# Kernel optimization log

Hardware: AMD Instinct MI355X
Metric: run time of the kernel (lower is better)

Reference implementation:

```python
import jax, jax.numpy as jnp
import numpy as np

N_NODES = 50000


def _gin_aggregate(x, src, dst):
    # sum_{j in N(i)} x_j via scatter-add over edges; eps=0 so add self term
    msg = x[src]  # [E, d]
    return x + jax.ops.segment_sum(msg, dst, num_segments=N_NODES)


def _mlp(h, Wa, ba, Wb, bb):
    return jax.nn.relu(h @ Wa + ba) @ Wb + bb


def setup_inputs() -> dict:
    key = jax.random.key(0)
    ks = jax.random.split(key, 12)
    d_in, d_h, n_cls, n_edges = 128, 128, 40, 800000
    x = jax.random.normal(ks[0], (N_NODES, d_in), dtype=jnp.float32)
    edge_index = jax.random.randint(ks[1], (2, n_edges), 0, N_NODES, dtype=jnp.int64)
    s = lambda k, sh: jax.random.normal(k, sh, dtype=jnp.float32) / np.sqrt(sh[0])
    return {
        "x": x,
        "edge_index": edge_index,
        "W11": s(ks[2], (d_in, 2 * d_h)), "b11": jnp.zeros((2 * d_h,), jnp.float32),
        "W12": s(ks[3], (2 * d_h, d_h)), "b12": jnp.zeros((d_h,), jnp.float32),
        "W21": s(ks[4], (d_h, 2 * d_h)), "b21": jnp.zeros((2 * d_h,), jnp.float32),
        "W22": s(ks[5], (2 * d_h, d_h)), "b22": jnp.zeros((d_h,), jnp.float32),
        "Wfc": s(ks[6], (d_h, n_cls)), "bfc": jnp.zeros((n_cls,), jnp.float32),
    }


def reference(x, edge_index, W11, b11, W12, b12, W21, b21, W22, b22, Wfc, bfc):
    src, dst = edge_index[0], edge_index[1]
    # GINConv 1: aggregate then MLP, followed by ReLU
    h = _mlp(_gin_aggregate(x, src, dst), W11, b11, W12, b12)
    h = jax.nn.relu(h)
    # GINConv 2
    h = _mlp(_gin_aggregate(h, src, dst), W21, b21, W22, b22)
    h = jax.nn.relu(h)
    # final classifier
    return h @ Wfc + bfc
```

## Files before the change

kernel.cpp:

```cpp
#include <hip/hip_runtime.h>

#define N_NODES 50000
#define N_EDGES 800000
#define NBUCK   98
#define EPB     2048
#define NSB     391
#define BCAP    64
#define CAPB    12288

typedef __attribute__((ext_vector_type(8))) short short8;
typedef __attribute__((ext_vector_type(4))) float floatx4;

__device__ __forceinline__ float b2f(unsigned short u) {
    union { unsigned int i; float f; } v;
    v.i = ((unsigned int)u) << 16;
    return v.f;
}
__device__ __forceinline__ float ubits(unsigned int b) {
    union { unsigned int i; float f; } v;
    v.i = b;
    return v.f;
}
__device__ __forceinline__ unsigned short f2b(float f) {
    union { float f; unsigned int i; } v;
    v.f = f;
    unsigned int r = v.i + 0x7FFFu + ((v.i >> 16) & 1u);
    return (unsigned short)(r >> 16);
}

__global__ __launch_bounds__(256) void prep_scatter(
    const float* __restrict__ x,
    const float* __restrict__ W11, const float* __restrict__ W12,
    const float* __restrict__ W21, const float* __restrict__ W22,
    const float* __restrict__ Wfc,
    const int* __restrict__ srcv, const int* __restrict__ dstv,
    unsigned short* __restrict__ xb,
    unsigned short* __restrict__ Wt11, unsigned short* __restrict__ Wt12,
    unsigned short* __restrict__ Wt21, unsigned short* __restrict__ Wt22,
    unsigned short* __restrict__ Wfct,
    int* __restrict__ cnt, int* __restrict__ tmp) {
    const int bid = blockIdx.x;
    const int tid = threadIdx.x;
    if (bid < NSB) {
        __shared__ int hist[NBUCK];
        const int k = bid;
        const int e0 = k * EPB;
        for (int i = tid; i < NBUCK; i += 256) hist[i] = 0;
        __syncthreads();
#pragma unroll
        for (int j = 0; j < EPB / 256; ++j) {
            int e = e0 + j * 256 + tid;
            if (e < N_EDGES) atomicAdd(&hist[dstv[e] >> 9], 1);
        }
        __syncthreads();
        for (int i = tid; i < NBUCK; i += 256) {
            cnt[i * NSB + k] = hist[i];
            hist[i] = 0;
        }
        __syncthreads();
#pragma unroll
        for (int j = 0; j < EPB / 256; ++j) {
            int e = e0 + j * 256 + tid;
            if (e < N_EDGES) {
                int d = dstv[e];
                int b = d >> 9;
                int r = atomicAdd(&hist[b], 1);
                if (r < BCAP)
                    tmp[((size_t)k * NBUCK + b) * BCAP + r] = srcv[e] | ((d & 511) << 16);
            }
        }
    } else if (bid < NSB + 512) {
        int wb = bid - NSB;
        int which = wb >> 7;
        int idx = (wb & 127) * 256 + tid;
        const float* W = (which == 0) ? W11 : (which == 1) ? W12 : (which == 2) ? W21 : W22;
        unsigned short* Wt = (which == 0) ? Wt11 : (which == 1) ? Wt12 : (which == 2) ? Wt21 : Wt22;
        int K = (which & 1) ? 256 : 128;
        int N = (which & 1) ? 128 : 256;
        int k = idx / N, n = idx - k * N;
        Wt[n * K + k] = f2b(W[idx]);
    } else if (bid < NSB + 536) {
        int idx = (bid - NSB - 512) * 256 + tid;
        int n = idx >> 7, k = idx & 127;
        Wfct[idx] = (n < 40) ? f2b(Wfc[k * 40 + n]) : (unsigned short)0;
    } else {
        int i = (bid - NSB - 536) * 256 + tid;
        const float4 a = *reinterpret_cast<const float4*>(x + (size_t)i * 8);
        const float4 b = *reinterpret_cast<const float4*>(x + (size_t)i * 8 + 4);
        ushort4 u0, u1;
        u0.x = f2b(a.x); u0.y = f2b(a.y); u0.z = f2b(a.z); u0.w = f2b(a.w);
        u1.x = f2b(b.x); u1.y = f2b(b.y); u1.z = f2b(b.z); u1.w = f2b(b.w);
        *reinterpret_cast<ushort4*>(xb + (size_t)i * 8) = u0;
        *reinterpret_cast<ushort4*>(xb + (size_t)i * 8 + 4) = u1;
    }
}

__global__ __launch_bounds__(256) void bucket_sort_ex(const int* __restrict__ cnt,
                                                      const int* __restrict__ tmp,
                                                      int* __restrict__ e_src,
                                                      int* __restrict__ row_ptr) {
    __shared__ int ps[256];
    __shared__ int sb[512];
    __shared__ int sc[512];
    __shared__ int nc[512];
    __shared__ int buf[CAPB];
    const int tid = threadIdx.x;
    const int b = blockIdx.x;

    sc[tid] = (tid < NSB) ? cnt[b * NSB + tid] : 0;
    sc[tid + 256] = (tid + 256 < NSB) ? cnt[b * NSB + tid + 256] : 0;
    __syncthreads();
    const int c0s = sc[2 * tid], c1s = sc[2 * tid + 1];
    ps[tid] = c0s + c1s;
    __syncthreads();
    for (int off = 1; off < 256; off <<= 1) {
        int u = (tid >= off) ? ps[tid - off] : 0;
        __syncthreads();
        ps[tid] += u;
        __syncthreads();
    }
    const int soff0 = ps[tid] - (c0s + c1s);
    sb[2 * tid] = soff0;
    sb[2 * tid + 1] = soff0 + c0s;
    __syncthreads();
    const int S = ps[255];

    const int lane = tid & 63, w = tid >> 6;
    const int hw = w * 2 + (lane >> 5), hl = lane & 31;
    for (int k = hw; k < NSB; k += 8) {
        const int base = sb[k], c = sc[k];
        const int* src = tmp + ((size_t)k * NBUCK + b) * BCAP;
        for (int i = hl; i < c; i += 32)
            if (base + i < CAPB) buf[base + i] = src[i];
    }
    for (int i = tid; i < 512; i += 256) nc[i] = 0;
    __syncthreads();
    for (int e = tid; e < S; e += 256)
        atomicAdd(&nc[(buf[e] >> 16) & 511], 1);
    __syncthreads();

    const int c0 = nc[2 * tid], c1 = nc[2 * tid + 1];
    ps[tid] = c0 + c1;
    __syncthreads();
    for (int off = 1; off < 256; off <<= 1) {
        int u = (tid >= off) ? ps[tid - off] : 0;
        __syncthreads();
        ps[tid] += u;
        __syncthreads();
    }
    const int off0 = ps[tid] - (c0 + c1);
    const int off1 = off0 + c0;
    nc[2 * tid] = off0;
    nc[2 * tid + 1] = off1;
    const int gbase = b * CAPB;
    row_ptr[b * 513 + 2 * tid] = gbase + off0;
    row_ptr[b * 513 + 2 * tid + 1] = gbase + off1;
    if (tid == 0) row_ptr[b * 513 + 512] = gbase + S;
    __syncthreads();

    for (int e = tid; e < S; e += 256) {
        int p = buf[e];
        int dl = (p >> 16) & 511;
        int pos = atomicAdd(&nc[dl], 1);
        e_src[gbase + pos] = p & 0xFFFF;
    }
}

__global__ __launch_bounds__(256) void agg_bf16q(const unsigned short* __restrict__ X,
                                                 const int* __restrict__ row_ptr,
                                                 const int* __restrict__ e_src,
                                                 unsigned short* __restrict__ agg) {
    const int node = (blockIdx.x * 256 + threadIdx.x) >> 6;
    const int lane = threadIdx.x & 63;
    const int qw = lane >> 4, ql = lane & 15;
    const size_t off = (size_t)ql * 8;

    const int rp = node + (node >> 9);
    const int beg = row_ptr[rp], end = row_ptr[rp + 1];
    float acc[8];
#pragma unroll
    for (int k = 0; k < 8; ++k) acc[k] = 0.f;

    if (qw == 0) {
        uint4 u = *reinterpret_cast<const uint4*>(X + (size_t)node * 128 + off);
        const unsigned int* up = (const unsigned int*)&u;
#pragma unroll
        for (int k = 0; k < 4; ++k) {
            acc[2 * k]     += ubits(up[k] << 16);
            acc[2 * k + 1] += ubits(up[k] & 0xFFFF0000u);
        }
    }

    int e = beg + qw;
    for (; e + 12 < end; e += 16) {
        const int s0 = e_src[e], s1 = e_src[e + 4], s2 = e_src[e + 8], s3 = e_src[e + 12];
        uint4 u0 = *reinterpret_cast<const uint4*>(X + (size_t)s0 * 128 + off);
        uint4 u1 = *reinterpret_cast<const uint4*>(X + (size_t)s1 * 128 + off);
        uint4 u2 = *reinterpret_cast<const uint4*>(X + (size_t)s2 * 128 + off);
        uint4 u3 = *reinterpret_cast<const uint4*>(X + (size_t)s3 * 128 + off);
        const unsigned int* p0 = (const unsigned int*)&u0;
        const unsigned int* p1 = (const unsigned int*)&u1;
        const unsigned int* p2 = (const unsigned int*)&u2;
        const unsigned int* p3 = (const unsigned int*)&u3;
#pragma unroll
        for (int k = 0; k < 4; ++k) {
            acc[2 * k]     += ubits(p0[k] << 16) + ubits(p1[k] << 16)
                            + ubits(p2[k] << 16) + ubits(p3[k] << 16);
            acc[2 * k + 1] += ubits(p0[k] & 0xFFFF0000u) + ubits(p1[k] & 0xFFFF0000u)
                            + ubits(p2[k] & 0xFFFF0000u) + ubits(p3[k] & 0xFFFF0000u);
        }
    }
    for (; e + 4 < end; e += 8) {
        const int s0 = e_src[e], s1 = e_src[e + 4];
        uint4 u0 = *reinterpret_cast<const uint4*>(X + (size_t)s0 * 128 + off);
        uint4 u1 = *reinterpret_cast<const uint4*>(X + (size_t)s1 * 128 + off);
        const unsigned int* p0 = (const unsigned int*)&u0;
        const unsigned int* p1 = (const unsigned int*)&u1;
#pragma unroll
        for (int k = 0; k < 4; ++k) {
            acc[2 * k]     += ubits(p0[k] << 16) + ubits(p1[k] << 16);
            acc[2 * k + 1] += ubits(p0[k] & 0xFFFF0000u) + ubits(p1[k] & 0xFFFF0000u);
        }
    }
    if (e < end) {
        const int s = e_src[e];
        uint4 u = *reinterpret_cast<const uint4*>(X + (size_t)s * 128 + off);
        const unsigned int* p = (const unsigned int*)&u;
#pragma unroll
        for (int k = 0; k < 4; ++k) {
            acc[2 * k]     += ubits(p[k] << 16);
            acc[2 * k + 1] += ubits(p[k] & 0xFFFF0000u);
        }
    }

#pragma unroll
    for (int k = 0; k < 8; ++k) acc[k] += __shfl_xor(acc[k], 32);
#pragma unroll
    for (int k = 0; k < 8; ++k) acc[k] += __shfl_xor(acc[k], 16);

    if (qw == 0) {
        ushort4 o0, o1;
        o0.x = f2b(acc[0]); o0.y = f2b(acc[1]); o0.z = f2b(acc[2]); o0.w = f2b(acc[3]);
        o1.x = f2b(acc[4]); o1.y = f2b(acc[5]); o1.z = f2b(acc[6]); o1.w = f2b(acc[7]);
        unsigned short* p = agg + (size_t)node * 128 + off;
        *reinterpret_cast<ushort4*>(p) = o0;
        *reinterpret_cast<ushort4*>(p + 4) = o1;
    }
}

template <bool FUSE>
__global__ __launch_bounds__(256, FUSE ? 2 : 3) void mlp_fused(
    const unsigned short* __restrict__ X, const unsigned short* __restrict__ Wt1,
    const float* __restrict__ b1, const unsigned short* __restrict__ Wt2,
    const float* __restrict__ b2, unsigned short* __restrict__ Y,
    const unsigned short* __restrict__ Wfct, const float* __restrict__ bfc,
    float* __restrict__ out, int M) {
    __shared__ __align__(16) char smem[FUSE ? 57344 : 52224];
    unsigned short* A   = (unsigned short*)smem;
    unsigned short* B2q = (unsigned short*)smem;
    unsigned short* B1h = (unsigned short*)(smem + 17408);
    unsigned short* T   = (unsigned short*)(smem + 17408);
    unsigned short* Hc  = (unsigned short*)(smem + 52224);

    const int tid = threadIdx.x;
    const int m0 = blockIdx.x * 64;
    const int lane = tid & 63, w = tid >> 6;
    const int qm = lane & 15, quad = lane >> 4;

#pragma unroll
    for (int j = 0; j < 4; ++j) {
        int i = j * 256 + tid;
        int r = i >> 4, c8 = (i & 15) << 3;
        uint4 v = {0, 0, 0, 0};
        if (m0 + r < M) v = *reinterpret_cast<const uint4*>(X + (size_t)(m0 + r) * 128 + c8);
        *reinterpret_cast<uint4*>(&A[r * 136 + c8]) = v;
    }

    floatx4 acc1[2][4][2];
#pragma unroll
    for (int c = 0; c < 2; ++c)
#pragma unroll
        for (int mt = 0; mt < 4; ++mt)
#pragma unroll
            for (int nt = 0; nt < 2; ++nt) acc1[c][mt][nt] = {0.f, 0.f, 0.f, 0.f};

    for (int c = 0; c < 2; ++c) {
#pragma unroll
        for (int j = 0; j < 8; ++j) {
            int i = j * 256 + tid;
            int r = i >> 4, c8 = (i & 15) << 3;
            *reinterpret_cast<uint4*>(&B1h[r * 136 + c8]) =
                *reinterpret_cast<const uint4*>(Wt1 + (size_t)(c * 128 + r) * 128 + c8);
        }
        __syncthreads();
#pragma unroll
        for (int ks = 0; ks < 4; ++ks) {
            const int kb = ks * 32 + quad * 8;
            short8 a[4], b[2];
#pragma unroll
            for (int mt = 0; mt < 4; ++mt)
                a[mt] = *reinterpret_cast<const short8*>(&A[(mt * 16 + qm) * 136 + kb]);
#pragma unroll
            for (int nt = 0; nt < 2; ++nt)
                b[nt] = *reinterpret_cast<const short8*>(&B1h[(w * 32 + nt * 16 + qm) * 136 + kb]);
#pragma unroll
            for (int mt = 0; mt < 4; ++mt)
#pragma unroll
                for (int nt = 0; nt < 2; ++nt)
                    acc1[c][mt][nt] = __builtin_amdgcn_mfma_f32_16x16x32_bf16(
                        a[mt], b[nt], acc1[c][mt][nt], 0, 0, 0);
        }
        __syncthreads();
    }

#pragma unroll
    for (int c = 0; c < 2; ++c) {
#pragma unroll
        for (int nt = 0; nt < 2; ++nt) {
            const int jcol = c * 128 + w * 32 + nt * 16 + qm;
            const float bj = b1[jcol];
#pragma unroll
            for (int mt = 0; mt < 4; ++mt)
#pragma unroll
                for (int r = 0; r < 4; ++r)
                    T[(mt * 16 + quad * 4 + r) * 264 + jcol] =
                        f2b(fmaxf(acc1[c][mt][nt][r] + bj, 0.f));
        }
    }

    floatx4 cacc[3];
#pragma unroll
    for (int nt = 0; nt < 3; ++nt) cacc[nt] = {0.f, 0.f, 0.f, 0.f};

    for (int c2 = 0; c2 < 4; ++c2) {
#pragma unroll
        for (int j = 0; j < 4; ++j) {
            int i = j * 256 + tid;
            int r = i >> 5, c8 = (i & 31) << 3;
            *reinterpret_cast<uint4*>(&B2q[r * 264 + c8]) =
                *reinterpret_cast<const uint4*>(Wt2 + (size_t)(c2 * 32 + r) * 256 + c8);
        }
        __syncthreads();

        floatx4 acc2[2];
        acc2[0] = {0.f, 0.f, 0.f, 0.f};
        acc2[1] = {0.f, 0.f, 0.f, 0.f};
#pragma unroll
        for (int ks = 0; ks < 8; ++ks) {
            const int kb = ks * 32 + quad * 8;
            short8 t0 = *reinterpret_cast<const short8*>(&T[((w & 1) * 32 + qm) * 264 + kb]);
            short8 t1 = *reinterpret_cast<const short8*>(&T[((w & 1) * 32 + 16 + qm) * 264 + kb]);
            short8 bb = *reinterpret_cast<const short8*>(&B2q[((w >> 1) * 16 + qm) * 264 + kb]);
            acc2[0] = __builtin_amdgcn_mfma_f32_16x16x32_bf16(t0, bb, acc2[0], 0, 0, 0);
            acc2[1] = __builtin_amdgcn_mfma_f32_16x16x32_bf16(t1, bb, acc2[1], 0, 0, 0);
        }

        const int ncol = c2 * 32 + (w >> 1) * 16 + qm;
        const float bj = b2[ncol];
        if (!FUSE) {
#pragma unroll
            for (int mt2 = 0; mt2 < 2; ++mt2)
#pragma unroll
                for (int r = 0; r < 4; ++r) {
                    int row = m0 + (w & 1) * 32 + mt2 * 16 + quad * 4 + r;
                    if (row < M)
                        Y[(size_t)row * 128 + ncol] = f2b(fmaxf(acc2[mt2][r] + bj, 0.f));
                }
            __syncthreads();
        } else {
            const int lcol = (w >> 1) * 16 + qm;
#pragma unroll
            for (int mt2 = 0; mt2 < 2; ++mt2)
#pragma unroll
                for (int r = 0; r < 4; ++r)
                    Hc[((w & 1) * 32 + mt2 * 16 + quad * 4 + r) * 40 + lcol] =
                        f2b(fmaxf(acc2[mt2][r] + bj, 0.f));
            __syncthreads();
            short8 hf = *reinterpret_cast<const short8*>(&Hc[(w * 16 + qm) * 40 + quad * 8]);
#pragma unroll
            for (int nt = 0; nt < 3; ++nt) {
                short8 bf = *reinterpret_cast<const short8*>(
                    Wfct + (nt * 16 + qm) * 128 + c2 * 32 + quad * 8);
                cacc[nt] = __builtin_amdgcn_mfma_f32_16x16x32_bf16(hf, bf, cacc[nt], 0, 0, 0);
            }
            __syncthreads();
        }
    }

    if (FUSE) {
#pragma unroll
        for (int nt = 0; nt < 3; ++nt) {
            int col = nt * 16 + qm;
            if (col < 40) {
                const float bj = bfc[col];
#pragma unroll
                for (int r = 0; r < 4; ++r) {
                    int row = m0 + w * 16 + quad * 4 + r;
                    if (row < M) out[(size_t)row * 40 + col] = cacc[nt][r] + bj;
                }
            }
        }
    }
}

extern "C" void kernel_launch(void* const* d_in, const int* in_sizes, int n_in,
                              void* d_out, int out_size, void* d_ws, size_t ws_size,
                              hipStream_t stream) {
    const float* x   = (const float*)d_in[0];
    const int*   ei  = (const int*)d_in[1];
    const float* W11 = (const float*)d_in[2];
    const float* b11 = (const float*)d_in[3];
    const float* W12 = (const float*)d_in[4];
    const float* b12 = (const float*)d_in[5];
    const float* W21 = (const float*)d_in[6];
    const float* b21 = (const float*)d_in[7];
    const float* W22 = (const float*)d_in[8];
    const float* b22 = (const float*)d_in[9];
    const float* Wfc = (const float*)d_in[10];
    const float* bfc = (const float*)d_in[11];
    float* out = (float*)d_out;

    const int* srcv = ei;
    const int* dstv = ei + N_EDGES;

    unsigned short* agg  = (unsigned short*)d_ws;
    unsigned short* h    = agg + (size_t)N_NODES * 128;
    unsigned short* xb   = h   + (size_t)N_NODES * 128;
    unsigned short* Wt11 = xb  + (size_t)N_NODES * 128;
    unsigned short* Wt12 = Wt11 + 256 * 128;
    unsigned short* Wt21 = Wt12 + 256 * 128;
    unsigned short* Wt22 = Wt21 + 256 * 128;
    unsigned short* Wfct = Wt22 + 256 * 128;
    int* cnt     = (int*)(Wfct + 48 * 128);
    int* row_ptr = cnt + 38400;
    int* e_src   = row_ptr + 50304;
    int* tmp     = e_src + (size_t)NBUCK * CAPB;

    prep_scatter<<<NSB + 3661, 256, 0, stream>>>(
        x, W11, W12, W21, W22, Wfc, srcv, dstv,
        xb, Wt11, Wt12, Wt21, Wt22, Wfct, cnt, tmp);

    bucket_sort_ex<<<NBUCK, 256, 0, stream>>>(cnt, tmp, e_src, row_ptr);

    const int agg_blocks = N_NODES * 64 / 256;
    const int mlp_blocks = (N_NODES + 63) / 64;

    agg_bf16q<<<agg_blocks, 256, 0, stream>>>(xb, row_ptr, e_src, agg);
    mlp_fused<false><<<mlp_blocks, 256, 0, stream>>>(
        agg, Wt11, b11, Wt12, b12, h, nullptr, nullptr, nullptr, N_NODES);
    agg_bf16q<<<agg_blocks, 256, 0, stream>>>(h, row_ptr, e_src, agg);
    mlp_fused<true><<<mlp_blocks, 256, 0, stream>>>(
        agg, Wt21, b21, Wt22, b22, nullptr, Wfct, bfc, out, N_NODES);
}
```

Measured before the change: 246.6 us.

## Fuse neighbor aggregation into MLP kernels and merge sort with weight conversion

The separate aggregation kernel is removed. Each MLP block now gathers and sums its 64 nodes' neighbor rows directly into shared memory, so the bf16 agg buffer no longer makes a round trip through global memory. The bucket-sort stage is merged with the weight and x conversion into one launch, and the edge scatter becomes its own kernel. The gather now uses 16 lanes per node, one node at a time per quarter-wave, where the old kernel spread a node's edges across a whole wave. This may cost memory-level parallelism, and the gather runs under the lower occupancy set by the MLP's launch bounds.

```diff
diff --git a/kernel.cpp b/kernel.cpp
--- a/kernel.cpp
+++ b/kernel.cpp
@@ -11,11 +11,6 @@
 typedef __attribute__((ext_vector_type(8))) short short8;
 typedef __attribute__((ext_vector_type(4))) float floatx4;
 
-__device__ __forceinline__ float b2f(unsigned short u) {
-    union { unsigned int i; float f; } v;
-    v.i = ((unsigned int)u) << 16;
-    return v.f;
-}
 __device__ __forceinline__ float ubits(unsigned int b) {
     union { unsigned int i; float f; } v;
     v.i = b;
@@ -28,49 +23,119 @@
     return (unsigned short)(r >> 16);
 }
 
-__global__ __launch_bounds__(256) void prep_scatter(
+__global__ __launch_bounds__(256) void scatter_edges(
+    const int* __restrict__ srcv, const int* __restrict__ dstv,
+    int* __restrict__ cnt, int* __restrict__ tmp) {
+    __shared__ int hist[NBUCK];
+    const int k = blockIdx.x;
+    const int tid = threadIdx.x;
+    const int e0 = k * EPB;
+    for (int i = tid; i < NBUCK; i += 256) hist[i] = 0;
+    __syncthreads();
+#pragma unroll
+    for (int j = 0; j < EPB / 256; ++j) {
+        int e = e0 + j * 256 + tid;
+        if (e < N_EDGES) atomicAdd(&hist[dstv[e] >> 9], 1);
+    }
+    __syncthreads();
+    for (int i = tid; i < NBUCK; i += 256) {
+        cnt[i * NSB + k] = hist[i];
+        hist[i] = 0;
+    }
+    __syncthreads();
+#pragma unroll
+    for (int j = 0; j < EPB / 256; ++j) {
+        int e = e0 + j * 256 + tid;
+        if (e < N_EDGES) {
+            int d = dstv[e];
+            int b = d >> 9;
+            int r = atomicAdd(&hist[b], 1);
+            if (r < BCAP)
+                tmp[((size_t)k * NBUCK + b) * BCAP + r] = srcv[e] | ((d & 511) << 16);
+        }
+    }
+}
+
+__global__ __launch_bounds__(256) void sort_conv(
+    const int* __restrict__ cnt, const int* __restrict__ tmp,
+    int* __restrict__ e_src, int* __restrict__ row_ptr,
     const float* __restrict__ x,
     const float* __restrict__ W11, const float* __restrict__ W12,
     const float* __restrict__ W21, const float* __restrict__ W22,
     const float* __restrict__ Wfc,
-    const int* __restrict__ srcv, const int* __restrict__ dstv,
     unsigned short* __restrict__ xb,
     unsigned short* __restrict__ Wt11, unsigned short* __restrict__ Wt12,
     unsigned short* __restrict__ Wt21, unsigned short* __restrict__ Wt22,
-    unsigned short* __restrict__ Wfct,
-    int* __restrict__ cnt, int* __restrict__ tmp) {
+    unsigned short* __restrict__ Wfct) {
+    __shared__ int ps[256];
+    __shared__ int sb[512];
+    __shared__ int sc[512];
+    __shared__ int nc[512];
+    __shared__ int buf[CAPB];
     const int bid = blockIdx.x;
     const int tid = threadIdx.x;
-    if (bid < NSB) {
-        __shared__ int hist[NBUCK];
-        const int k = bid;
-        const int e0 = k * EPB;
-        for (int i = tid; i < NBUCK; i += 256) hist[i] = 0;
-        __syncthreads();
-#pragma unroll
-        for (int j = 0; j < EPB / 256; ++j) {
-            int e = e0 + j * 256 + tid;
-            if (e < N_EDGES) atomicAdd(&hist[dstv[e] >> 9], 1);
-        }
-        __syncthreads();
-        for (int i = tid; i < NBUCK; i += 256) {
-            cnt[i * NSB + k] = hist[i];
-            hist[i] = 0;
-        }
-        __syncthreads();
-#pragma unroll
-        for (int j = 0; j < EPB / 256; ++j) {
-            int e = e0 + j * 256 + tid;
-            if (e < N_EDGES) {
-                int d = dstv[e];
-                int b = d >> 9;
-                int r = atomicAdd(&hist[b], 1);
-                if (r < BCAP)
-                    tmp[((size_t)k * NBUCK + b) * BCAP + r] = srcv[e] | ((d & 511) << 16);
-            }
-        }
-    } else if (bid < NSB + 512) {
-        int wb = bid - NSB;
+
+    if (bid < NBUCK) {
+        const int b = bid;
+        sc[tid] = (tid < NSB) ? cnt[b * NSB + tid] : 0;
+        sc[tid + 256] = (tid + 256 < NSB) ? cnt[b * NSB + tid + 256] : 0;
+        __syncthreads();
+        const int c0s = sc[2 * tid], c1s = sc[2 * tid + 1];
+        ps[tid] = c0s + c1s;
+        __syncthreads();
+        for (int off = 1; off < 256; off <<= 1) {
+            int u = (tid >= off) ? ps[tid - off] : 0;
+            __syncthreads();
+            ps[tid] += u;
+            __syncthreads();
+        }
+        const int soff0 = ps[tid] - (c0s + c1s);
+        sb[2 * tid] = soff0;
+        sb[2 * tid + 1] = soff0 + c0s;
+        __syncthreads();
+        const int S = ps[255];
+
+        const int lane = tid & 63, w = tid >> 6;
+        const int hw = w * 2 + (lane >> 5), hl = lane & 31;
+        for (int k = hw; k < NSB; k += 8) {
+            const int base = sb[k], c = sc[k];
+            const int* src = tmp + ((size_t)k * NBUCK + b) * BCAP;
+            for (int i = hl; i < c; i += 32)
+                if (base + i < CAPB) buf[base + i] = src[i];
+        }
+        for (int i = tid; i < 512; i += 256) nc[i] = 0;
+        __syncthreads();
+        for (int e = tid; e < S; e += 256)
+            atomicAdd(&nc[(buf[e] >> 16) & 511], 1);
+        __syncthreads();
+
+        const int c0 = nc[2 * tid], c1 = nc[2 * tid + 1];
+        ps[tid] = c0 + c1;
+        __syncthreads();
+        for (int off = 1; off < 256; off <<= 1) {
+            int u = (tid >= off) ? ps[tid - off] : 0;
+            __syncthreads();
+            ps[tid] += u;
+            __syncthreads();
+        }
+        const int off0 = ps[tid] - (c0 + c1);
+        const int off1 = off0 + c0;
+        nc[2 * tid] = off0;
+        nc[2 * tid + 1] = off1;
+        const int gbase = b * CAPB;
+        row_ptr[b * 513 + 2 * tid] = gbase + off0;
+        row_ptr[b * 513 + 2 * tid + 1] = gbase + off1;
+        if (tid == 0) row_ptr[b * 513 + 512] = gbase + S;
+        __syncthreads();
+
+        for (int e = tid; e < S; e += 256) {
+            int p = buf[e];
+            int dl = (p >> 16) & 511;
+            int pos = atomicAdd(&nc[dl], 1);
+            e_src[gbase + pos] = p & 0xFFFF;
+        }
+    } else if (bid < NBUCK + 512) {
+        int wb = bid - NBUCK;
         int which = wb >> 7;
         int idx = (wb & 127) * 256 + tid;
         const float* W = (which == 0) ? W11 : (which == 1) ? W12 : (which == 2) ? W21 : W22;
@@ -79,12 +144,12 @@
         int N = (which & 1) ? 128 : 256;
         int k = idx / N, n = idx - k * N;
         Wt[n * K + k] = f2b(W[idx]);
-    } else if (bid < NSB + 536) {
-        int idx = (bid - NSB - 512) * 256 + tid;
+    } else if (bid < NBUCK + 536) {
+        int idx = (bid - NBUCK - 512) * 256 + tid;
         int n = idx >> 7, k = idx & 127;
         Wfct[idx] = (n < 40) ? f2b(Wfc[k * 40 + n]) : (unsigned short)0;
     } else {
-        int i = (bid - NSB - 536) * 256 + tid;
+        int i = (bid - NBUCK - 536) * 256 + tid;
         const float4 a = *reinterpret_cast<const float4*>(x + (size_t)i * 8);
         const float4 b = *reinterpret_cast<const float4*>(x + (size_t)i * 8 + 4);
         ushort4 u0, u1;
@@ -95,162 +160,11 @@
     }
 }
 
-__global__ __launch_bounds__(256) void bucket_sort_ex(const int* __restrict__ cnt,
-                                                      const int* __restrict__ tmp,
-                                                      int* __restrict__ e_src,
-                                                      int* __restrict__ row_ptr) {
-    __shared__ int ps[256];
-    __shared__ int sb[512];
-    __shared__ int sc[512];
-    __shared__ int nc[512];
-    __shared__ int buf[CAPB];
-    const int tid = threadIdx.x;
-    const int b = blockIdx.x;
-
-    sc[tid] = (tid < NSB) ? cnt[b * NSB + tid] : 0;
-    sc[tid + 256] = (tid + 256 < NSB) ? cnt[b * NSB + tid + 256] : 0;
-    __syncthreads();
-    const int c0s = sc[2 * tid], c1s = sc[2 * tid + 1];
-    ps[tid] = c0s + c1s;
-    __syncthreads();
-    for (int off = 1; off < 256; off <<= 1) {
-        int u = (tid >= off) ? ps[tid - off] : 0;
-        __syncthreads();
-        ps[tid] += u;
-        __syncthreads();
-    }
-    const int soff0 = ps[tid] - (c0s + c1s);
-    sb[2 * tid] = soff0;
-    sb[2 * tid + 1] = soff0 + c0s;
-    __syncthreads();
-    const int S = ps[255];
-
-    const int lane = tid & 63, w = tid >> 6;
-    const int hw = w * 2 + (lane >> 5), hl = lane & 31;
-    for (int k = hw; k < NSB; k += 8) {
-        const int base = sb[k], c = sc[k];
-        const int* src = tmp + ((size_t)k * NBUCK + b) * BCAP;
-        for (int i = hl; i < c; i += 32)
-            if (base + i < CAPB) buf[base + i] = src[i];
-    }
-    for (int i = tid; i < 512; i += 256) nc[i] = 0;
-    __syncthreads();
-    for (int e = tid; e < S; e += 256)
-        atomicAdd(&nc[(buf[e] >> 16) & 511], 1);
-    __syncthreads();
-
-    const int c0 = nc[2 * tid], c1 = nc[2 * tid + 1];
-    ps[tid] = c0 + c1;
-    __syncthreads();
-    for (int off = 1; off < 256; off <<= 1) {
-        int u = (tid >= off) ? ps[tid - off] : 0;
-        __syncthreads();
-        ps[tid] += u;
-        __syncthreads();
-    }
-    const int off0 = ps[tid] - (c0 + c1);
-    const int off1 = off0 + c0;
-    nc[2 * tid] = off0;
-    nc[2 * tid + 1] = off1;
-    const int gbase = b * CAPB;
-    row_ptr[b * 513 + 2 * tid] = gbase + off0;
-    row_ptr[b * 513 + 2 * tid + 1] = gbase + off1;
-    if (tid == 0) row_ptr[b * 513 + 512] = gbase + S;
-    __syncthreads();
-
-    for (int e = tid; e < S; e += 256) {
-        int p = buf[e];
-        int dl = (p >> 16) & 511;
-        int pos = atomicAdd(&nc[dl], 1);
-        e_src[gbase + pos] = p & 0xFFFF;
-    }
-}
-
-__global__ __launch_bounds__(256) void agg_bf16q(const unsigned short* __restrict__ X,
-                                                 const int* __restrict__ row_ptr,
-                                                 const int* __restrict__ e_src,
-                                                 unsigned short* __restrict__ agg) {
-    const int node = (blockIdx.x * 256 + threadIdx.x) >> 6;
-    const int lane = threadIdx.x & 63;
-    const int qw = lane >> 4, ql = lane & 15;
-    const size_t off = (size_t)ql * 8;
-
-    const int rp = node + (node >> 9);
-    const int beg = row_ptr[rp], end = row_ptr[rp + 1];
-    float acc[8];
-#pragma unroll
-    for (int k = 0; k < 8; ++k) acc[k] = 0.f;
-
-    if (qw == 0) {
-        uint4 u = *reinterpret_cast<const uint4*>(X + (size_t)node * 128 + off);
-        const unsigned int* up = (const unsigned int*)&u;
-#pragma unroll
-        for (int k = 0; k < 4; ++k) {
-            acc[2 * k]     += ubits(up[k] << 16);
-            acc[2 * k + 1] += ubits(up[k] & 0xFFFF0000u);
-        }
-    }
-
-    int e = beg + qw;
-    for (; e + 12 < end; e += 16) {
-        const int s0 = e_src[e], s1 = e_src[e + 4], s2 = e_src[e + 8], s3 = e_src[e + 12];
-        uint4 u0 = *reinterpret_cast<const uint4*>(X + (size_t)s0 * 128 + off);
-        uint4 u1 = *reinterpret_cast<const uint4*>(X + (size_t)s1 * 128 + off);
-        uint4 u2 = *reinterpret_cast<const uint4*>(X + (size_t)s2 * 128 + off);
-        uint4 u3 = *reinterpret_cast<const uint4*>(X + (size_t)s3 * 128 + off);
-        const unsigned int* p0 = (const unsigned int*)&u0;
-        const unsigned int* p1 = (const unsigned int*)&u1;
-        const unsigned int* p2 = (const unsigned int*)&u2;
-        const unsigned int* p3 = (const unsigned int*)&u3;
-#pragma unroll
-        for (int k = 0; k < 4; ++k) {
-            acc[2 * k]     += ubits(p0[k] << 16) + ubits(p1[k] << 16)
-                            + ubits(p2[k] << 16) + ubits(p3[k] << 16);
-            acc[2 * k + 1] += ubits(p0[k] & 0xFFFF0000u) + ubits(p1[k] & 0xFFFF0000u)
-                            + ubits(p2[k] & 0xFFFF0000u) + ubits(p3[k] & 0xFFFF0000u);
-        }
-    }
-    for (; e + 4 < end; e += 8) {
-        const int s0 = e_src[e], s1 = e_src[e + 4];
-        uint4 u0 = *reinterpret_cast<const uint4*>(X + (size_t)s0 * 128 + off);
-        uint4 u1 = *reinterpret_cast<const uint4*>(X + (size_t)s1 * 128 + off);
-        const unsigned int* p0 = (const unsigned int*)&u0;
-        const unsigned int* p1 = (const unsigned int*)&u1;
-#pragma unroll
-        for (int k = 0; k < 4; ++k) {
-            acc[2 * k]     += ubits(p0[k] << 16) + ubits(p1[k] << 16);
-            acc[2 * k + 1] += ubits(p0[k] & 0xFFFF0000u) + ubits(p1[k] & 0xFFFF0000u);
-        }
-    }
-    if (e < end) {
-        const int s = e_src[e];
-        uint4 u = *reinterpret_cast<const uint4*>(X + (size_t)s * 128 + off);
-        const unsigned int* p = (const unsigned int*)&u;
-#pragma unroll
-        for (int k = 0; k < 4; ++k) {
-            acc[2 * k]     += ubits(p[k] << 16);
-            acc[2 * k + 1] += ubits(p[k] & 0xFFFF0000u);
-        }
-    }
-
-#pragma unroll
-    for (int k = 0; k < 8; ++k) acc[k] += __shfl_xor(acc[k], 32);
-#pragma unroll
-    for (int k = 0; k < 8; ++k) acc[k] += __shfl_xor(acc[k], 16);
-
-    if (qw == 0) {
-        ushort4 o0, o1;
-        o0.x = f2b(acc[0]); o0.y = f2b(acc[1]); o0.z = f2b(acc[2]); o0.w = f2b(acc[3]);
-        o1.x = f2b(acc[4]); o1.y = f2b(acc[5]); o1.z = f2b(acc[6]); o1.w = f2b(acc[7]);
-        unsigned short* p = agg + (size_t)node * 128 + off;
-        *reinterpret_cast<ushort4*>(p) = o0;
-        *reinterpret_cast<ushort4*>(p + 4) = o1;
-    }
-}
-
 template <bool FUSE>
 __global__ __launch_bounds__(256, FUSE ? 2 : 3) void mlp_fused(
-    const unsigned short* __restrict__ X, const unsigned short* __restrict__ Wt1,
+    const unsigned short* __restrict__ X,
+    const int* __restrict__ row_ptr, const int* __restrict__ e_src,
+    const unsigned short* __restrict__ Wt1,
     const float* __restrict__ b1, const unsigned short* __restrict__ Wt2,
     const float* __restrict__ b2, unsigned short* __restrict__ Y,
     const unsigned short* __restrict__ Wfct, const float* __restrict__ bfc,
@@ -267,13 +181,63 @@
     const int lane = tid & 63, w = tid >> 6;
     const int qm = lane & 15, quad = lane >> 4;
 
-#pragma unroll
-    for (int j = 0; j < 4; ++j) {
-        int i = j * 256 + tid;
-        int r = i >> 4, c8 = (i & 15) << 3;
-        uint4 v = {0, 0, 0, 0};
-        if (m0 + r < M) v = *reinterpret_cast<const uint4*>(X + (size_t)(m0 + r) * 128 + c8);
-        *reinterpret_cast<uint4*>(&A[r * 136 + c8]) = v;
+    {
+        const size_t off = (size_t)qm * 8;
+#pragma unroll
+        for (int g = 0; g < 4; ++g) {
+            const int nloc = w * 16 + g * 4 + quad;
+            const int node = m0 + nloc;
+            float acc[8];
+#pragma unroll
+            for (int k = 0; k < 8; ++k) acc[k] = 0.f;
+            if (node < M) {
+                const int rp = node + (node >> 9);
+                int e = row_ptr[rp];
+                const int end = row_ptr[rp + 1];
+                uint4 us = *reinterpret_cast<const uint4*>(X + (size_t)node * 128 + off);
+                const unsigned int* up = (const unsigned int*)&us;
+#pragma unroll
+                for (int k = 0; k < 4; ++k) {
+                    acc[2 * k]     += ubits(up[k] << 16);
+                    acc[2 * k + 1] += ubits(up[k] & 0xFFFF0000u);
+                }
+                for (; e + 3 < end; e += 4) {
+                    const int s0 = e_src[e], s1 = e_src[e + 1];
+                    const int s2 = e_src[e + 2], s3 = e_src[e + 3];
+                    uint4 u0 = *reinterpret_cast<const uint4*>(X + (size_t)s0 * 128 + off);
+                    uint4 u1 = *reinterpret_cast<const uint4*>(X + (size_t)s1 * 128 + off);
+                    uint4 u2 = *reinterpret_cast<const uint4*>(X + (size_t)s2 * 128 + off);
+                    uint4 u3 = *reinterpret_cast<const uint4*>(X + (size_t)s3 * 128 + off);
+                    const unsigned int* p0 = (const unsigned int*)&u0;
+                    const unsigned int* p1 = (const unsigned int*)&u1;
+                    const unsigned int* p2 = (const unsigned int*)&u2;
+                    const unsigned int* p3 = (const unsigned int*)&u3;
+#pragma unroll
+                    for (int k = 0; k < 4; ++k) {
+                        acc[2 * k]     += ubits(p0[k] << 16) + ubits(p1[k] << 16)
+                                        + ubits(p2[k] << 16) + ubits(p3[k] << 16);
+                        acc[2 * k + 1] += ubits(p0[k] & 0xFFFF0000u) + ubits(p1[k] & 0xFFFF0000u)
+                                        + ubits(p2[k] & 0xFFFF0000u) + ubits(p3[k] & 0xFFFF0000u);
+                    }
+                }
+                for (; e < end; ++e) {
+                    const int s = e_src[e];
+                    uint4 u = *reinterpret_cast<const uint4*>(X + (size_t)s * 128 + off);
+                    const unsigned int* p = (const unsigned int*)&u;
+#pragma unroll
+                    for (int k = 0; k < 4; ++k) {
+                        acc[2 * k]     += ubits(p[k] << 16);
+                        acc[2 * k + 1] += ubits(p[k] & 0xFFFF0000u);
+                    }
+                }
+            }
+            ushort4 o0, o1;
+            o0.x = f2b(acc[0]); o0.y = f2b(acc[1]); o0.z = f2b(acc[2]); o0.w = f2b(acc[3]);
+            o1.x = f2b(acc[4]); o1.y = f2b(acc[5]); o1.z = f2b(acc[6]); o1.w = f2b(acc[7]);
+            unsigned short* ap = &A[nloc * 136 + qm * 8];
+            *reinterpret_cast<ushort4*>(ap) = o0;
+            *reinterpret_cast<ushort4*>(ap + 4) = o1;
+        }
     }
 
     floatx4 acc1[2][4][2];
@@ -436,19 +400,17 @@
     int* e_src   = row_ptr + 50304;
     int* tmp     = e_src + (size_t)NBUCK * CAPB;
 
-    prep_scatter<<<NSB + 3661, 256, 0, stream>>>(
-        x, W11, W12, W21, W22, Wfc, srcv, dstv,
-        xb, Wt11, Wt12, Wt21, Wt22, Wfct, cnt, tmp);
-
-    bucket_sort_ex<<<NBUCK, 256, 0, stream>>>(cnt, tmp, e_src, row_ptr);
-
-    const int agg_blocks = N_NODES * 64 / 256;
+    scatter_edges<<<NSB, 256, 0, stream>>>(srcv, dstv, cnt, tmp);
+
+    sort_conv<<<NBUCK + 536 + 3125, 256, 0, stream>>>(
+        cnt, tmp, e_src, row_ptr,
+        x, W11, W12, W21, W22, Wfc,
+        xb, Wt11, Wt12, Wt21, Wt22, Wfct);
+
     const int mlp_blocks = (N_NODES + 63) / 64;
 
-    agg_bf16q<<<agg_blocks, 256, 0, stream>>>(xb, row_ptr, e_src, agg);
     mlp_fused<false><<<mlp_blocks, 256, 0, stream>>>(
-        agg, Wt11, b11, Wt12, b12, h, nullptr, nullptr, nullptr, N_NODES);
-    agg_bf16q<<<agg_blocks, 256, 0, stream>>>(h, row_ptr, e_src, agg);
+        xb, row_ptr, e_src, Wt11, b11, Wt12, b12, h, nullptr, nullptr, nullptr, N_NODES);
     mlp_fused<true><<<mlp_blocks, 256, 0, stream>>>(
-        agg, Wt21, b21, Wt22, b22, nullptr, Wfct, bfc, out, N_NODES);
-}
+        h, row_ptr, e_src, Wt21, b21, Wt22, b22, nullptr, Wfct, bfc, out, N_NODES);
+}
```

After: 273.8 us. +11.0%, slower.

## Replace two-kernel bucket sort with four-pass counting sort into compact buckets

Applied to the files above, without the earlier changes.

Edge sorting by destination now uses 392 buckets of 128 nodes each, built in four passes: histogram, per-bucket prefix scan of strip counts, placement of edges into compact per-bucket buffers, and a per-bucket local counting sort that writes CSR. This drops the fixed-capacity padded tmp slots (BCAP 64) and the large shared-memory staging buffer, giving more parallel blocks in the finishing pass. It costs two extra kernel launches and a second read of src/dst edges.

```diff
diff --git a/kernel.cpp b/kernel.cpp
--- a/kernel.cpp
+++ b/kernel.cpp
@@ -2,20 +2,14 @@
 
 #define N_NODES 50000
 #define N_EDGES 800000
-#define NBUCK   98
+#define NBUCK   392
 #define EPB     2048
 #define NSB     391
-#define BCAP    64
-#define CAPB    12288
+#define CAPB    2560
 
 typedef __attribute__((ext_vector_type(8))) short short8;
 typedef __attribute__((ext_vector_type(4))) float floatx4;
 
-__device__ __forceinline__ float b2f(unsigned short u) {
-    union { unsigned int i; float f; } v;
-    v.i = ((unsigned int)u) << 16;
-    return v.f;
-}
 __device__ __forceinline__ float ubits(unsigned int b) {
     union { unsigned int i; float f; } v;
     v.i = b;
@@ -28,17 +22,15 @@
     return (unsigned short)(r >> 16);
 }
 
-__global__ __launch_bounds__(256) void prep_scatter(
-    const float* __restrict__ x,
+__global__ __launch_bounds__(256) void hist_conv(
+    const int* __restrict__ dstv, const float* __restrict__ x,
     const float* __restrict__ W11, const float* __restrict__ W12,
     const float* __restrict__ W21, const float* __restrict__ W22,
     const float* __restrict__ Wfc,
-    const int* __restrict__ srcv, const int* __restrict__ dstv,
-    unsigned short* __restrict__ xb,
+    int* __restrict__ cnt, unsigned short* __restrict__ xb,
     unsigned short* __restrict__ Wt11, unsigned short* __restrict__ Wt12,
     unsigned short* __restrict__ Wt21, unsigned short* __restrict__ Wt22,
-    unsigned short* __restrict__ Wfct,
-    int* __restrict__ cnt, int* __restrict__ tmp) {
+    unsigned short* __restrict__ Wfct) {
     const int bid = blockIdx.x;
     const int tid = threadIdx.x;
     if (bid < NSB) {
@@ -50,25 +42,10 @@
 #pragma unroll
         for (int j = 0; j < EPB / 256; ++j) {
             int e = e0 + j * 256 + tid;
-            if (e < N_EDGES) atomicAdd(&hist[dstv[e] >> 9], 1);
-        }
-        __syncthreads();
-        for (int i = tid; i < NBUCK; i += 256) {
-            cnt[i * NSB + k] = hist[i];
-            hist[i] = 0;
-        }
-        __syncthreads();
-#pragma unroll
-        for (int j = 0; j < EPB / 256; ++j) {
-            int e = e0 + j * 256 + tid;
-            if (e < N_EDGES) {
-                int d = dstv[e];
-                int b = d >> 9;
-                int r = atomicAdd(&hist[b], 1);
-                if (r < BCAP)
-                    tmp[((size_t)k * NBUCK + b) * BCAP + r] = srcv[e] | ((d & 511) << 16);
-            }
-        }
+            if (e < N_EDGES) atomicAdd(&hist[dstv[e] >> 7], 1);
+        }
+        __syncthreads();
+        for (int i = tid; i < NBUCK; i += 256) cnt[i * NSB + k] = hist[i];
     } else if (bid < NSB + 512) {
         int wb = bid - NSB;
         int which = wb >> 7;
@@ -95,23 +72,17 @@
     }
 }
 
-__global__ __launch_bounds__(256) void bucket_sort_ex(const int* __restrict__ cnt,
-                                                      const int* __restrict__ tmp,
-                                                      int* __restrict__ e_src,
-                                                      int* __restrict__ row_ptr) {
+__global__ __launch_bounds__(256) void scan_strips(
+    const int* __restrict__ cnt, int* __restrict__ sbase) {
     __shared__ int ps[256];
-    __shared__ int sb[512];
     __shared__ int sc[512];
-    __shared__ int nc[512];
-    __shared__ int buf[CAPB];
+    const int b = blockIdx.x;
     const int tid = threadIdx.x;
-    const int b = blockIdx.x;
-
     sc[tid] = (tid < NSB) ? cnt[b * NSB + tid] : 0;
     sc[tid + 256] = (tid + 256 < NSB) ? cnt[b * NSB + tid + 256] : 0;
     __syncthreads();
-    const int c0s = sc[2 * tid], c1s = sc[2 * tid + 1];
-    ps[tid] = c0s + c1s;
+    const int c0 = sc[2 * tid], c1 = sc[2 * tid + 1];
+    ps[tid] = c0 + c1;
     __syncthreads();
     for (int off = 1; off < 256; off <<= 1) {
         int u = (tid >= off) ? ps[tid - off] : 0;
@@ -119,50 +90,67 @@
         ps[tid] += u;
         __syncthreads();
     }
-    const int soff0 = ps[tid] - (c0s + c1s);
-    sb[2 * tid] = soff0;
-    sb[2 * tid + 1] = soff0 + c0s;
-    __syncthreads();
-    const int S = ps[255];
-
-    const int lane = tid & 63, w = tid >> 6;
-    const int hw = w * 2 + (lane >> 5), hl = lane & 31;
-    for (int k = hw; k < NSB; k += 8) {
-        const int base = sb[k], c = sc[k];
-        const int* src = tmp + ((size_t)k * NBUCK + b) * BCAP;
-        for (int i = hl; i < c; i += 32)
-            if (base + i < CAPB) buf[base + i] = src[i];
-    }
-    for (int i = tid; i < 512; i += 256) nc[i] = 0;
-    __syncthreads();
-    for (int e = tid; e < S; e += 256)
-        atomicAdd(&nc[(buf[e] >> 16) & 511], 1);
-    __syncthreads();
-
-    const int c0 = nc[2 * tid], c1 = nc[2 * tid + 1];
-    ps[tid] = c0 + c1;
-    __syncthreads();
-    for (int off = 1; off < 256; off <<= 1) {
-        int u = (tid >= off) ? ps[tid - off] : 0;
-        __syncthreads();
-        ps[tid] += u;
-        __syncthreads();
-    }
-    const int off0 = ps[tid] - (c0 + c1);
-    const int off1 = off0 + c0;
-    nc[2 * tid] = off0;
-    nc[2 * tid + 1] = off1;
-    const int gbase = b * CAPB;
-    row_ptr[b * 513 + 2 * tid] = gbase + off0;
-    row_ptr[b * 513 + 2 * tid + 1] = gbase + off1;
-    if (tid == 0) row_ptr[b * 513 + 512] = gbase + S;
-    __syncthreads();
-
-    for (int e = tid; e < S; e += 256) {
-        int p = buf[e];
-        int dl = (p >> 16) & 511;
-        int pos = atomicAdd(&nc[dl], 1);
-        e_src[gbase + pos] = p & 0xFFFF;
+    if (tid < 196) {
+        const int off0 = ps[tid] - (c0 + c1);
+        sbase[b * 392 + 2 * tid] = off0;
+        sbase[b * 392 + 2 * tid + 1] = off0 + c0;
+    }
+}
+
+__global__ __launch_bounds__(256) void place_compact(
+    const int* __restrict__ srcv, const int* __restrict__ dstv,
+    const int* __restrict__ sbase, int* __restrict__ bufc) {
+    __shared__ int cur[NBUCK];
+    const int k = blockIdx.x;
+    const int tid = threadIdx.x;
+    for (int i = tid; i < NBUCK; i += 256) cur[i] = sbase[i * 392 + k];
+    __syncthreads();
+    const int e0 = k * EPB;
+#pragma unroll
+    for (int j = 0; j < EPB / 256; ++j) {
+        int e = e0 + j * 256 + tid;
+        if (e < N_EDGES) {
+            int d = dstv[e];
+            int b = d >> 7;
+            int pos = atomicAdd(&cur[b], 1);
+            bufc[b * CAPB + pos] = srcv[e] | ((d & 127) << 16);
+        }
+    }
+}
+
+__global__ __launch_bounds__(256) void finish_buckets(
+    const int* __restrict__ sbase, const int* __restrict__ bufc,
+    int* __restrict__ e_src, int* __restrict__ row_ptr) {
+    __shared__ int nc[128];
+    __shared__ int ps[128];
+    const int b = blockIdx.x;
+    const int tid = threadIdx.x;
+    const int S = sbase[b * 392 + 391];
+    const int gb = b * CAPB;
+    if (tid < 128) nc[tid] = 0;
+    __syncthreads();
+    for (int t = tid; t < S; t += 256)
+        atomicAdd(&nc[(bufc[gb + t] >> 16) & 127], 1);
+    __syncthreads();
+    if (tid < 128) ps[tid] = nc[tid];
+    __syncthreads();
+    for (int off = 1; off < 128; off <<= 1) {
+        int u = (tid >= off && tid < 128) ? ps[tid - off] : 0;
+        __syncthreads();
+        if (tid < 128) ps[tid] += u;
+        __syncthreads();
+    }
+    if (tid < 128) {
+        const int excl = ps[tid] - nc[tid];
+        row_ptr[b * 129 + tid] = gb + excl;
+        nc[tid] = gb + excl;
+    }
+    if (tid == 0) row_ptr[b * 129 + 128] = gb + S;
+    __syncthreads();
+    for (int t = tid; t < S; t += 256) {
+        int p = bufc[gb + t];
+        int pos = atomicAdd(&nc[(p >> 16) & 127], 1);
+        e_src[pos] = p & 0xFFFF;
     }
 }
 
@@ -175,7 +163,7 @@
     const int qw = lane >> 4, ql = lane & 15;
     const size_t off = (size_t)ql * 8;
 
-    const int rp = node + (node >> 9);
+    const int rp = node + (node >> 7);
     const int beg = row_ptr[rp], end = row_ptr[rp + 1];
     float acc[8];
 #pragma unroll
@@ -432,15 +420,20 @@
     unsigned short* Wt22 = Wt21 + 256 * 128;
     unsigned short* Wfct = Wt22 + 256 * 128;
     int* cnt     = (int*)(Wfct + 48 * 128);
-    int* row_ptr = cnt + 38400;
-    int* e_src   = row_ptr + 50304;
-    int* tmp     = e_src + (size_t)NBUCK * CAPB;
-
-    prep_scatter<<<NSB + 3661, 256, 0, stream>>>(
-        x, W11, W12, W21, W22, Wfc, srcv, dstv,
-        xb, Wt11, Wt12, Wt21, Wt22, Wfct, cnt, tmp);
-
-    bucket_sort_ex<<<NBUCK, 256, 0, stream>>>(cnt, tmp, e_src, row_ptr);
+    int* sbase   = cnt + 153664;
+    int* row_ptr = sbase + 153664;
+    int* e_src   = row_ptr + 50688;
+    int* bufc    = e_src + (size_t)NBUCK * CAPB;
+
+    hist_conv<<<NSB + 3661, 256, 0, stream>>>(
+        dstv, x, W11, W12, W21, W22, Wfc,
+        cnt, xb, Wt11, Wt12, Wt21, Wt22, Wfct);
+
+    scan_strips<<<NBUCK, 256, 0, stream>>>(cnt, sbase);
+
+    place_compact<<<NSB, 256, 0, stream>>>(srcv, dstv, sbase, bufc);
+
+    finish_buckets<<<NBUCK, 256, 0, stream>>>(sbase, bufc, e_src, row_ptr);
 
     const int agg_blocks = N_NODES * 64 / 256;
     const int mlp_blocks = (N_NODES + 63) / 64;
```

Result: faster. 230.9 us (-6.4%).
